# Optimization experiments

Measured on AMD Instinct MI355X. Metric: run time of the kernel, lower is better.

Reference implementation:

```python
import jax, jax.numpy as jnp
import numpy as np

BLOCK = 32          # per_1x32 microscaling block size along K
FP4_MAX = 6.0       # largest magnitude representable in e2m1
FP4_EMAX = 2.0      # exponent of largest fp4 binade (4..6)


def _quant_dequant_mxfp4(x):
    """Simulate MXFP4 (e2m1 elements, shared power-of-two E8M0 scale per 1x32
    block along the last dim): quantize then dequantize. x: [..., K], K % 32 == 0."""
    shape = x.shape
    xb = x.reshape(*shape[:-1], shape[-1] // BLOCK, BLOCK)
    amax = jnp.max(jnp.abs(xb), axis=-1, keepdims=True)
    # shared scale: 2^(floor(log2(amax)) - emax) so the block max lands in the top binade
    exp = jnp.floor(jnp.log2(jnp.maximum(amax, jnp.finfo(x.dtype).tiny))) - FP4_EMAX
    scale = jnp.where(amax > 0, jnp.exp2(exp), jnp.ones_like(amax))
    q = jnp.clip(xb / scale, -FP4_MAX, FP4_MAX)
    aq = jnp.abs(q)
    # e2m1 ulp: 0.5 on [0,2), 1 on [2,4), 2 on [4,6]
    lsb = jnp.where(aq < 2.0, 0.5, jnp.where(aq < 4.0, 1.0, 2.0))
    qr = jnp.round(q / lsb) * lsb  # round-to-nearest-even onto the fp4 grid
    return (qr * scale).reshape(shape)


def setup_inputs() -> dict:
    key = jax.random.key(0)
    k1, k2, k3 = jax.random.split(key, 3)
    B, S, K, N = 4, 2048, 2048, 2048
    inp = jax.random.normal(k1, (B, S, K), dtype=jnp.float32)
    weight = jax.random.normal(k2, (N, K), dtype=jnp.float32) * (1.0 / np.sqrt(K))
    bias = jax.random.normal(k3, (N,), dtype=jnp.float32) * 0.02
    return {"input": inp, "weight": weight, "bias": bias}


def reference(input, weight, bias):
    # both activation and weight are fake-quantized to MXFP4 per 1x32 blocks
    # along the contraction (in_features) dim, then a standard GEMM + bias.
    orig_shape = input.shape
    a = _quant_dequant_mxfp4(input.reshape(-1, orig_shape[-1]))  # [M, K]
    w = _quant_dequant_mxfp4(weight)                              # [N, K]
    out = jnp.einsum("mk,nk->mn", a, w) + bias
    return out.reshape(*orig_shape[:-1], weight.shape[0])
```

## Files before the change

### kernel.cpp

```cpp
#include <hip/hip_runtime.h>
#include <cstdint>


#define BM 128
#define BN 128
#define BK 256

typedef float floatx16 __attribute__((ext_vector_type(16)));
typedef int intx8 __attribute__((ext_vector_type(8)));

#define GLOBAL_AS __attribute__((address_space(1)))
#define LDS_AS __attribute__((address_space(3)))


__device__ __forceinline__ int enc1(float x, float inv) {
    float q = x * inv;
    q = fminf(fmaxf(q, -6.0f), 6.0f);
    int s = (int)(__float_as_uint(q) >> 31) << 3;
    float aq = fabsf(q);
    float ilsb = aq < 2.0f ? 2.0f : (aq < 4.0f ? 1.0f : 0.5f);
    float lsb  = aq < 2.0f ? 0.5f : (aq < 4.0f ? 1.0f : 2.0f);
    float ar = rintf(aq * ilsb) * lsb;
    int c;
    if (ar < 2.0f)      c = (int)(ar * 2.0f);
    else if (ar < 4.0f) c = 2 + (int)ar;
    else                c = 4 + (int)(ar * 0.5f);
    return c | s;
}

__global__ void quant_mxfp4_v4(const float* __restrict__ A, uint8_t* __restrict__ Aq,
                               uint8_t* __restrict__ AscT,
                               const float* __restrict__ W, uint8_t* __restrict__ Wq,
                               uint8_t* __restrict__ WscT,
                               long na4, long ntot4, int s4, long Mr, long Nr) {
    long t = (long)blockIdx.x * 256 + threadIdx.x;
    if (t >= ntot4) return;
    const float* src; uint8_t* dq; uint8_t* ds; long idx; long rows;
    if (t < na4) { src = A; dq = Aq; ds = AscT; idx = t; rows = Mr; }
    else         { src = W; dq = Wq; ds = WscT; idx = t - na4; rows = Nr; }

    float4 f = ((const float4*)src)[idx];
    float amax = fmaxf(fmaxf(fabsf(f.x), fabsf(f.y)),
                       fmaxf(fabsf(f.z), fabsf(f.w)));
    amax = fmaxf(amax, __shfl_xor(amax, 1));
    amax = fmaxf(amax, __shfl_xor(amax, 2));
    amax = fmaxf(amax, __shfl_xor(amax, 4));

    int ebits = (int)((__float_as_uint(amax) >> 23) & 0xff);
    int sb;
    float inv;
    if (amax > 0.0f) {
        sb = ebits - 2; if (sb < 0) sb = 0;
        inv = __uint_as_float((unsigned)((256 - ebits) & 255) << 23);
    } else {
        sb = 127;
        inv = 0.0f;
    }

    int c0 = enc1(f.x, inv), c1 = enc1(f.y, inv);
    int c2 = enc1(f.z, inv), c3 = enc1(f.w, inv);
    ((unsigned short*)dq)[idx] =
        (unsigned short)(c0 | (c1 << 4) | (c2 << 8) | (c3 << 12));
    if ((idx & 7) == 0) {
        long m  = idx >> s4;
        int  kb = (int)((idx & ((1L << s4) - 1)) >> 3);
        ds[(size_t)kb * rows + m] = (uint8_t)sb;
    }
}


__global__ __launch_bounds__(256, 2) void gemm_fp4_v8(
        const uint8_t* __restrict__ Aq, const uint8_t* __restrict__ AscT,
        const uint8_t* __restrict__ Wq, const uint8_t* __restrict__ WscT,
        const float* __restrict__ bias, float* __restrict__ C,
        int M, int N, int K) {
    __shared__ __align__(16) uint8_t sA[2][BM * 128];
    __shared__ __align__(16) uint8_t sB[2][BN * 128];

    const int tid = threadIdx.x;
    const int lane = tid & 63;
    const int w = tid >> 6;
    const int wr = w >> 1;
    const int wc = w & 1;
    const int row32 = lane & 31;
    const int q2 = lane >> 5;

    const int id = blockIdx.x;
    const int g = id & 7, h = id >> 3;
    const int by = g + 8 * (h & 7);
    const int bx = h >> 3;
    const int m0 = by * BM;
    const int n0 = bx * BN;
    const int KB2 = K >> 1;
    const int NT = K / BK;

    const int rA = wr * 64 + row32;
    const int rB = wc * 64 + row32;
    const int swz = row32 & 7;

    floatx16 acc[2][2];
#pragma unroll
    for (int i = 0; i < 2; i++)
#pragma unroll
        for (int j = 0; j < 2; j++)
#pragma unroll
            for (int r = 0; r < 16; r++) acc[i][j][r] = 0.f;

    auto stage = [&](int tt) {
        const int bb = tt & 1;
        const int kb = tt * 128;
#pragma unroll
        for (int it = 0; it < 4; ++it) {
            int idx = it * 256 + tid;
            int row = idx >> 3, c = idx & 7;
            int gc = c ^ (row & 7);
            const uint8_t* src = Aq + (size_t)(m0 + row) * KB2 + kb + gc * 16;
            __builtin_amdgcn_global_load_lds((GLOBAL_AS void*)src,
                (LDS_AS void*)(&sA[bb][idx * 16]), 16, 0, 0);
        }
#pragma unroll
        for (int it = 0; it < 4; ++it) {
            int idx = it * 256 + tid;
            int row = idx >> 3, c = idx & 7;
            int gc = c ^ (row & 7);
            const uint8_t* src = Wq + (size_t)(n0 + row) * KB2 + kb + gc * 16;
            __builtin_amdgcn_global_load_lds((GLOBAL_AS void*)src,
                (LDS_AS void*)(&sB[bb][idx * 16]), 16, 0, 0);
        }
    };

    stage(0);
    stage(1);
    asm volatile("s_waitcnt vmcnt(8)" ::: "memory");
    __builtin_amdgcn_sched_barrier(0);
    __builtin_amdgcn_s_barrier();

    for (int t = 0; t < NT; ++t) {
        const int p = t & 1;
        const uint8_t* pa = sA[p];
        const uint8_t* pb = sB[p];

        int sa[4][2], sb[4][2];
#pragma unroll
        for (int ks = 0; ks < 4; ++ks)
#pragma unroll
            for (int i = 0; i < 2; ++i) {
                sa[ks][i] = (int)AscT[(size_t)(8 * t + 2 * ks + q2) * M +
                                      m0 + wr * 64 + i * 32 + row32];
                sb[ks][i] = (int)WscT[(size_t)(8 * t + 2 * ks + q2) * N +
                                      n0 + wc * 64 + i * 32 + row32];
            }

        int4 fa[4][2], fb[4][2];
#pragma unroll
        for (int ks = 0; ks < 4; ++ks) {
            int off = ((ks * 2 + q2) ^ swz) * 16;
#pragma unroll
            for (int i = 0; i < 2; ++i) {
                fa[ks][i] = *(const int4*)(pa + (rA + i * 32) * 128 + off);
                fb[ks][i] = *(const int4*)(pb + (rB + i * 32) * 128 + off);
            }
        }

        asm volatile("s_waitcnt lgkmcnt(0)" ::: "memory");
        __builtin_amdgcn_sched_barrier(0);
        __builtin_amdgcn_s_barrier();

        if (t + 2 < NT) stage(t + 2);

        if (t + 2 < NT) asm volatile("s_waitcnt vmcnt(8)" ::: "memory");
        else            asm volatile("s_waitcnt vmcnt(0)" ::: "memory");
        __builtin_amdgcn_sched_barrier(0);

        __builtin_amdgcn_s_setprio(1);
#pragma unroll
        for (int ks = 0; ks < 4; ++ks) {
            intx8 a0, a1, b0, b1;
            a0[0] = fa[ks][0].x; a0[1] = fa[ks][0].y; a0[2] = fa[ks][0].z; a0[3] = fa[ks][0].w;
            a1[0] = fa[ks][1].x; a1[1] = fa[ks][1].y; a1[2] = fa[ks][1].z; a1[3] = fa[ks][1].w;
            b0[0] = fb[ks][0].x; b0[1] = fb[ks][0].y; b0[2] = fb[ks][0].z; b0[3] = fb[ks][0].w;
            b1[0] = fb[ks][1].x; b1[1] = fb[ks][1].y; b1[2] = fb[ks][1].z; b1[3] = fb[ks][1].w;
#pragma unroll
            for (int z = 4; z < 8; ++z) { a0[z] = 0; a1[z] = 0; b0[z] = 0; b1[z] = 0; }
            acc[0][0] = __builtin_amdgcn_mfma_scale_f32_32x32x64_f8f6f4(
                a0, b0, acc[0][0], 4, 4, 0, sa[ks][0], 0, sb[ks][0]);
            acc[0][1] = __builtin_amdgcn_mfma_scale_f32_32x32x64_f8f6f4(
                a0, b1, acc[0][1], 4, 4, 0, sa[ks][0], 0, sb[ks][1]);
            acc[1][0] = __builtin_amdgcn_mfma_scale_f32_32x32x64_f8f6f4(
                a1, b0, acc[1][0], 4, 4, 0, sa[ks][1], 0, sb[ks][0]);
            acc[1][1] = __builtin_amdgcn_mfma_scale_f32_32x32x64_f8f6f4(
                a1, b1, acc[1][1], 4, 4, 0, sa[ks][1], 0, sb[ks][1]);
        }
        __builtin_amdgcn_s_setprio(0);

        if (t < NT - 1) {
            if (t + 2 < NT) asm volatile("s_waitcnt vmcnt(8)" ::: "memory");
            else            asm volatile("s_waitcnt vmcnt(0)" ::: "memory");
            __builtin_amdgcn_sched_barrier(0);
            __builtin_amdgcn_s_barrier();
        }
    }

#pragma unroll
    for (int j = 0; j < 2; ++j) {
        int n = n0 + wc * 64 + j * 32 + row32;
        float bv = bias[n];
#pragma unroll
        for (int i = 0; i < 2; ++i) {
            int mb = m0 + wr * 64 + i * 32 + 4 * q2;
#pragma unroll
            for (int r = 0; r < 16; ++r) {
                int m = mb + (r & 3) + 8 * (r >> 2);
                C[(size_t)m * N + n] = acc[i][j][r] + bv;
            }
        }
    }
}


extern "C" void kernel_launch(void* const* d_in, const int* in_sizes, int n_in,
                              void* d_out, int out_size, void* d_ws, size_t ws_size,
                              hipStream_t stream) {
    const float* inp  = (const float*)d_in[0];
    const float* wgt  = (const float*)d_in[1];
    const float* bias = (const float*)d_in[2];
    float* out = (float*)d_out;

    const int N = in_sizes[2];
    const int K = in_sizes[1] / N;
    const long M = (long)in_sizes[0] / K;

    uint8_t* Aq4  = (uint8_t*)d_ws;
    uint8_t* Wq4  = Aq4 + (size_t)M * K / 2;
    uint8_t* AscT = Wq4 + (size_t)N * K / 2;
    uint8_t* WscT = AscT + (size_t)M * K / 32;

    int s4 = 0;
    while ((1 << s4) < (K >> 2)) ++s4;

    long na4   = (long)M * K / 4;
    long ntot4 = na4 + (long)N * K / 4;
    quant_mxfp4_v4<<<dim3((ntot4 + 255) / 256), dim3(256), 0, stream>>>(
        inp, Aq4, AscT, wgt, Wq4, WscT, na4, ntot4, s4, M, (long)N);

    dim3 grid((N / BN) * (int)(M / BM));
    gemm_fp4_v8<<<grid, dim3(256), 0, stream>>>(
        Aq4, AscT, Wq4, WscT, bias, out, (int)M, N, K);
}
```

Measured before the change: 152.6 us.

## Enlarge GEMM tile to 256x256 with 8 waves and packed scale layout

```diff
diff --git a/kernel.cpp b/kernel.cpp
--- a/kernel.cpp
+++ b/kernel.cpp
@@ -2,8 +2,8 @@
 #include <cstdint>
 
 
-#define BM 128
-#define BN 128
+#define BM 256
+#define BN 256
 #define BK 256
 
 typedef float floatx16 __attribute__((ext_vector_type(16)));
@@ -28,16 +28,16 @@
     return c | s;
 }
 
-__global__ void quant_mxfp4_v4(const float* __restrict__ A, uint8_t* __restrict__ Aq,
-                               uint8_t* __restrict__ AscT,
+__global__ void quant_mxfp4_v5(const float* __restrict__ A, uint8_t* __restrict__ Aq,
+                               uint8_t* __restrict__ Asc,
                                const float* __restrict__ W, uint8_t* __restrict__ Wq,
-                               uint8_t* __restrict__ WscT,
+                               uint8_t* __restrict__ Wsc,
                                long na4, long ntot4, int s4, long Mr, long Nr) {
     long t = (long)blockIdx.x * 256 + threadIdx.x;
     if (t >= ntot4) return;
     const float* src; uint8_t* dq; uint8_t* ds; long idx; long rows;
-    if (t < na4) { src = A; dq = Aq; ds = AscT; idx = t; rows = Mr; }
-    else         { src = W; dq = Wq; ds = WscT; idx = t - na4; rows = Nr; }
+    if (t < na4) { src = A; dq = Aq; ds = Asc; idx = t; rows = Mr; }
+    else         { src = W; dq = Wq; ds = Wsc; idx = t - na4; rows = Nr; }
 
     float4 f = ((const float4*)src)[idx];
     float amax = fmaxf(fmaxf(fabsf(f.x), fabsf(f.y)),
@@ -64,14 +64,83 @@
     if ((idx & 7) == 0) {
         long m  = idx >> s4;
         int  kb = (int)((idx & ((1L << s4) - 1)) >> 3);
-        ds[(size_t)kb * rows + m] = (uint8_t)sb;
-    }
-}
-
-
-__global__ __launch_bounds__(256, 2) void gemm_fp4_v8(
-        const uint8_t* __restrict__ Aq, const uint8_t* __restrict__ AscT,
-        const uint8_t* __restrict__ Wq, const uint8_t* __restrict__ WscT,
+        ds[((size_t)(kb >> 3) * rows + m) * 8 + (kb & 7)] = (uint8_t)sb;
+    }
+}
+
+
+#define GITER(T, CUR, NXT)                                                     \
+  {                                                                            \
+    const int p_ = (T) & 1;                                                    \
+    const uint8_t* pa_ = sA[p_];                                               \
+    const uint8_t* pb_ = sB[p_];                                               \
+    if ((T) + 1 < NT) {                                                        \
+      _Pragma("unroll") for (int mi = 0; mi < 4; ++mi)                         \
+        sgA[NXT][mi] = *(const uint2*)(Asc +                                   \
+            ((size_t)((T) + 1) * M + m0 + rA0 + mi * 32) * 8);                 \
+      _Pragma("unroll") for (int ni = 0; ni < 2; ++ni)                         \
+        sgB[NXT][ni] = *(const uint2*)(Wsc +                                   \
+            ((size_t)((T) + 1) * N + n0 + rB0 + ni * 32) * 8);                 \
+    }                                                                          \
+    __builtin_amdgcn_sched_barrier(0);                                         \
+    int4 fa_[4], fb_[2];                                                       \
+    _Pragma("unroll") for (int mi = 0; mi < 4; ++mi)                           \
+      fa_[mi] = *(const int4*)(pa_ + (rA0 + mi * 32) * 128 + (q2 ^ swz) * 16); \
+    _Pragma("unroll") for (int ni = 0; ni < 2; ++ni)                           \
+      fb_[ni] = *(const int4*)(pb_ + (rB0 + ni * 32) * 128 + (q2 ^ swz) * 16); \
+    __builtin_amdgcn_s_setprio(1);                                             \
+    _Pragma("unroll") for (int ks = 0; ks < 4; ++ks) {                         \
+      int4 na_[4], nb_[2];                                                     \
+      if (ks < 3) {                                                            \
+        const int off_ = (((ks + 1) * 2 + q2) ^ swz) * 16;                     \
+        _Pragma("unroll") for (int mi = 0; mi < 4; ++mi)                       \
+          na_[mi] = *(const int4*)(pa_ + (rA0 + mi * 32) * 128 + off_);        \
+        _Pragma("unroll") for (int ni = 0; ni < 2; ++ni)                       \
+          nb_[ni] = *(const int4*)(pb_ + (rB0 + ni * 32) * 128 + off_);        \
+      }                                                                        \
+      int sav_[4], sbv_[2];                                                    \
+      _Pragma("unroll") for (int mi = 0; mi < 4; ++mi)                         \
+        sav_[mi] = (int)(((ks < 2) ? (sgA[CUR][mi].x >> ((ks * 2 + q2) * 8))   \
+                   : (sgA[CUR][mi].y >> (((ks - 2) * 2 + q2) * 8))) & 0xffu);  \
+      _Pragma("unroll") for (int ni = 0; ni < 2; ++ni)                         \
+        sbv_[ni] = (int)(((ks < 2) ? (sgB[CUR][ni].x >> ((ks * 2 + q2) * 8))   \
+                   : (sgB[CUR][ni].y >> (((ks - 2) * 2 + q2) * 8))) & 0xffu);  \
+      intx8 b80_, b81_;                                                        \
+      b80_[0] = fb_[0].x; b80_[1] = fb_[0].y; b80_[2] = fb_[0].z;              \
+      b80_[3] = fb_[0].w; b80_[4] = 0; b80_[5] = 0; b80_[6] = 0; b80_[7] = 0;  \
+      b81_[0] = fb_[1].x; b81_[1] = fb_[1].y; b81_[2] = fb_[1].z;              \
+      b81_[3] = fb_[1].w; b81_[4] = 0; b81_[5] = 0; b81_[6] = 0; b81_[7] = 0;  \
+      _Pragma("unroll") for (int mi = 0; mi < 4; ++mi) {                       \
+        intx8 a8_;                                                             \
+        a8_[0] = fa_[mi].x; a8_[1] = fa_[mi].y; a8_[2] = fa_[mi].z;            \
+        a8_[3] = fa_[mi].w; a8_[4] = 0; a8_[5] = 0; a8_[6] = 0; a8_[7] = 0;    \
+        acc[mi][0] = __builtin_amdgcn_mfma_scale_f32_32x32x64_f8f6f4(          \
+            a8_, b80_, acc[mi][0], 4, 4, 0, sav_[mi], 0, sbv_[0]);             \
+        acc[mi][1] = __builtin_amdgcn_mfma_scale_f32_32x32x64_f8f6f4(          \
+            a8_, b81_, acc[mi][1], 4, 4, 0, sav_[mi], 0, sbv_[1]);             \
+      }                                                                        \
+      if (ks < 3) {                                                            \
+        _Pragma("unroll") for (int mi = 0; mi < 4; ++mi) fa_[mi] = na_[mi];    \
+        _Pragma("unroll") for (int ni = 0; ni < 2; ++ni) fb_[ni] = nb_[ni];    \
+      }                                                                        \
+    }                                                                          \
+    __builtin_amdgcn_s_setprio(0);                                             \
+    if ((T) + 1 < NT) {                                                        \
+      asm volatile("s_waitcnt lgkmcnt(0)" ::: "memory");                       \
+      __builtin_amdgcn_sched_barrier(0);                                       \
+      __builtin_amdgcn_s_barrier();                                            \
+      if ((T) + 2 < NT) stage((T) + 2);                                        \
+      __builtin_amdgcn_sched_barrier(0);                                       \
+      if ((T) + 2 < NT) asm volatile("s_waitcnt vmcnt(8)" ::: "memory");       \
+      else              asm volatile("s_waitcnt vmcnt(0)" ::: "memory");       \
+      __builtin_amdgcn_sched_barrier(0);                                       \
+      __builtin_amdgcn_s_barrier();                                            \
+    }                                                                          \
+  }
+
+__global__ __launch_bounds__(512, 2) void gemm_fp4_v9(
+        const uint8_t* __restrict__ Aq, const uint8_t* __restrict__ Asc,
+        const uint8_t* __restrict__ Wq, const uint8_t* __restrict__ Wsc,
         const float* __restrict__ bias, float* __restrict__ C,
         int M, int N, int K) {
     __shared__ __align__(16) uint8_t sA[2][BM * 128];
@@ -80,27 +149,27 @@
     const int tid = threadIdx.x;
     const int lane = tid & 63;
     const int w = tid >> 6;
-    const int wr = w >> 1;
-    const int wc = w & 1;
+    const int wr = w >> 2;
+    const int wc = w & 3;
     const int row32 = lane & 31;
     const int q2 = lane >> 5;
 
     const int id = blockIdx.x;
     const int g = id & 7, h = id >> 3;
-    const int by = g + 8 * (h & 7);
-    const int bx = h >> 3;
+    const int by = g * 4 + (h & 3);
+    const int bx = h >> 2;
     const int m0 = by * BM;
     const int n0 = bx * BN;
     const int KB2 = K >> 1;
     const int NT = K / BK;
 
-    const int rA = wr * 64 + row32;
-    const int rB = wc * 64 + row32;
+    const int rA0 = wr * 128 + row32;
+    const int rB0 = wc * 64 + row32;
     const int swz = row32 & 7;
 
-    floatx16 acc[2][2];
-#pragma unroll
-    for (int i = 0; i < 2; i++)
+    floatx16 acc[4][2];
+#pragma unroll
+    for (int i = 0; i < 4; i++)
 #pragma unroll
         for (int j = 0; j < 2; j++)
 #pragma unroll
@@ -111,7 +180,7 @@
         const int kb = tt * 128;
 #pragma unroll
         for (int it = 0; it < 4; ++it) {
-            int idx = it * 256 + tid;
+            int idx = it * 512 + tid;
             int row = idx >> 3, c = idx & 7;
             int gc = c ^ (row & 7);
             const uint8_t* src = Aq + (size_t)(m0 + row) * KB2 + kb + gc * 16;
@@ -120,7 +189,7 @@
         }
 #pragma unroll
         for (int it = 0; it < 4; ++it) {
-            int idx = it * 256 + tid;
+            int idx = it * 512 + tid;
             int row = idx >> 3, c = idx & 7;
             int gc = c ^ (row & 7);
             const uint8_t* src = Wq + (size_t)(n0 + row) * KB2 + kb + gc * 16;
@@ -129,89 +198,39 @@
         }
     };
 
+    uint2 sgA[2][4], sgB[2][2];
+
     stage(0);
+    __builtin_amdgcn_sched_barrier(0);
+#pragma unroll
+    for (int mi = 0; mi < 4; ++mi)
+        sgA[0][mi] = *(const uint2*)(Asc + ((size_t)0 * M + m0 + rA0 + mi * 32) * 8);
+#pragma unroll
+    for (int ni = 0; ni < 2; ++ni)
+        sgB[0][ni] = *(const uint2*)(Wsc + ((size_t)0 * N + n0 + rB0 + ni * 32) * 8);
+    __builtin_amdgcn_sched_barrier(0);
     stage(1);
+    __builtin_amdgcn_sched_barrier(0);
     asm volatile("s_waitcnt vmcnt(8)" ::: "memory");
     __builtin_amdgcn_sched_barrier(0);
     __builtin_amdgcn_s_barrier();
 
-    for (int t = 0; t < NT; ++t) {
-        const int p = t & 1;
-        const uint8_t* pa = sA[p];
-        const uint8_t* pb = sB[p];
-
-        int sa[4][2], sb[4][2];
-#pragma unroll
-        for (int ks = 0; ks < 4; ++ks)
-#pragma unroll
-            for (int i = 0; i < 2; ++i) {
-                sa[ks][i] = (int)AscT[(size_t)(8 * t + 2 * ks + q2) * M +
-                                      m0 + wr * 64 + i * 32 + row32];
-                sb[ks][i] = (int)WscT[(size_t)(8 * t + 2 * ks + q2) * N +
-                                      n0 + wc * 64 + i * 32 + row32];
-            }
-
-        int4 fa[4][2], fb[4][2];
-#pragma unroll
-        for (int ks = 0; ks < 4; ++ks) {
-            int off = ((ks * 2 + q2) ^ swz) * 16;
-#pragma unroll
-            for (int i = 0; i < 2; ++i) {
-                fa[ks][i] = *(const int4*)(pa + (rA + i * 32) * 128 + off);
-                fb[ks][i] = *(const int4*)(pb + (rB + i * 32) * 128 + off);
-            }
-        }
-
-        asm volatile("s_waitcnt lgkmcnt(0)" ::: "memory");
-        __builtin_amdgcn_sched_barrier(0);
-        __builtin_amdgcn_s_barrier();
-
-        if (t + 2 < NT) stage(t + 2);
-
-        if (t + 2 < NT) asm volatile("s_waitcnt vmcnt(8)" ::: "memory");
-        else            asm volatile("s_waitcnt vmcnt(0)" ::: "memory");
-        __builtin_amdgcn_sched_barrier(0);
-
-        __builtin_amdgcn_s_setprio(1);
-#pragma unroll
-        for (int ks = 0; ks < 4; ++ks) {
-            intx8 a0, a1, b0, b1;
-            a0[0] = fa[ks][0].x; a0[1] = fa[ks][0].y; a0[2] = fa[ks][0].z; a0[3] = fa[ks][0].w;
-            a1[0] = fa[ks][1].x; a1[1] = fa[ks][1].y; a1[2] = fa[ks][1].z; a1[3] = fa[ks][1].w;
-            b0[0] = fb[ks][0].x; b0[1] = fb[ks][0].y; b0[2] = fb[ks][0].z; b0[3] = fb[ks][0].w;
-            b1[0] = fb[ks][1].x; b1[1] = fb[ks][1].y; b1[2] = fb[ks][1].z; b1[3] = fb[ks][1].w;
-#pragma unroll
-            for (int z = 4; z < 8; ++z) { a0[z] = 0; a1[z] = 0; b0[z] = 0; b1[z] = 0; }
-            acc[0][0] = __builtin_amdgcn_mfma_scale_f32_32x32x64_f8f6f4(
-                a0, b0, acc[0][0], 4, 4, 0, sa[ks][0], 0, sb[ks][0]);
-            acc[0][1] = __builtin_amdgcn_mfma_scale_f32_32x32x64_f8f6f4(
-                a0, b1, acc[0][1], 4, 4, 0, sa[ks][0], 0, sb[ks][1]);
-            acc[1][0] = __builtin_amdgcn_mfma_scale_f32_32x32x64_f8f6f4(
-                a1, b0, acc[1][0], 4, 4, 0, sa[ks][1], 0, sb[ks][0]);
-            acc[1][1] = __builtin_amdgcn_mfma_scale_f32_32x32x64_f8f6f4(
-                a1, b1, acc[1][1], 4, 4, 0, sa[ks][1], 0, sb[ks][1]);
-        }
-        __builtin_amdgcn_s_setprio(0);
-
-        if (t < NT - 1) {
-            if (t + 2 < NT) asm volatile("s_waitcnt vmcnt(8)" ::: "memory");
-            else            asm volatile("s_waitcnt vmcnt(0)" ::: "memory");
-            __builtin_amdgcn_sched_barrier(0);
-            __builtin_amdgcn_s_barrier();
-        }
-    }
-
-#pragma unroll
-    for (int j = 0; j < 2; ++j) {
-        int n = n0 + wc * 64 + j * 32 + row32;
+    for (int t = 0; t < NT; t += 2) {
+        GITER(t, 0, 1);
+        GITER(t + 1, 1, 0);
+    }
+
+#pragma unroll
+    for (int ni = 0; ni < 2; ++ni) {
+        int n = n0 + wc * 64 + ni * 32 + row32;
         float bv = bias[n];
 #pragma unroll
-        for (int i = 0; i < 2; ++i) {
-            int mb = m0 + wr * 64 + i * 32 + 4 * q2;
+        for (int mi = 0; mi < 4; ++mi) {
+            int mb = m0 + wr * 128 + mi * 32 + 4 * q2;
 #pragma unroll
             for (int r = 0; r < 16; ++r) {
                 int m = mb + (r & 3) + 8 * (r >> 2);
-                C[(size_t)m * N + n] = acc[i][j][r] + bv;
+                C[(size_t)m * N + n] = acc[mi][ni][r] + bv;
             }
         }
     }
@@ -230,20 +249,20 @@
     const int K = in_sizes[1] / N;
     const long M = (long)in_sizes[0] / K;
 
-    uint8_t* Aq4  = (uint8_t*)d_ws;
-    uint8_t* Wq4  = Aq4 + (size_t)M * K / 2;
-    uint8_t* AscT = Wq4 + (size_t)N * K / 2;
-    uint8_t* WscT = AscT + (size_t)M * K / 32;
+    uint8_t* Aq4 = (uint8_t*)d_ws;
+    uint8_t* Wq4 = Aq4 + (size_t)M * K / 2;
+    uint8_t* Asc = Wq4 + (size_t)N * K / 2;
+    uint8_t* Wsc = Asc + (size_t)M * K / 32;
 
     int s4 = 0;
     while ((1 << s4) < (K >> 2)) ++s4;
 
     long na4   = (long)M * K / 4;
     long ntot4 = na4 + (long)N * K / 4;
-    quant_mxfp4_v4<<<dim3((ntot4 + 255) / 256), dim3(256), 0, stream>>>(
-        inp, Aq4, AscT, wgt, Wq4, WscT, na4, ntot4, s4, M, (long)N);
+    quant_mxfp4_v5<<<dim3((ntot4 + 255) / 256), dim3(256), 0, stream>>>(
+        inp, Aq4, Asc, wgt, Wq4, Wsc, na4, ntot4, s4, M, (long)N);
 
     dim3 grid((N / BN) * (int)(M / BM));
-    gemm_fp4_v8<<<grid, dim3(256), 0, stream>>>(
-        Aq4, AscT, Wq4, WscT, bias, out, (int)M, N, K);
-}
+    gemm_fp4_v9<<<grid, dim3(512), 0, stream>>>(
+        Aq4, Asc, Wq4, Wsc, bias, out, (int)M, N, K);
+}
```

Result: slower. 188.2 us (+23.3%).

## Pack per-tile scales into 8-byte groups and simplify GEMM pipeline

Applied to the files above, without the earlier changes.

```diff
diff --git a/kernel.cpp b/kernel.cpp
--- a/kernel.cpp
+++ b/kernel.cpp
@@ -28,16 +28,16 @@
     return c | s;
 }
 
-__global__ void quant_mxfp4_v4(const float* __restrict__ A, uint8_t* __restrict__ Aq,
-                               uint8_t* __restrict__ AscT,
+__global__ void quant_mxfp4_v5(const float* __restrict__ A, uint8_t* __restrict__ Aq,
+                               uint8_t* __restrict__ Asc,
                                const float* __restrict__ W, uint8_t* __restrict__ Wq,
-                               uint8_t* __restrict__ WscT,
+                               uint8_t* __restrict__ Wsc,
                                long na4, long ntot4, int s4, long Mr, long Nr) {
     long t = (long)blockIdx.x * 256 + threadIdx.x;
     if (t >= ntot4) return;
     const float* src; uint8_t* dq; uint8_t* ds; long idx; long rows;
-    if (t < na4) { src = A; dq = Aq; ds = AscT; idx = t; rows = Mr; }
-    else         { src = W; dq = Wq; ds = WscT; idx = t - na4; rows = Nr; }
+    if (t < na4) { src = A; dq = Aq; ds = Asc; idx = t; rows = Mr; }
+    else         { src = W; dq = Wq; ds = Wsc; idx = t - na4; rows = Nr; }
 
     float4 f = ((const float4*)src)[idx];
     float amax = fmaxf(fmaxf(fabsf(f.x), fabsf(f.y)),
@@ -64,14 +64,14 @@
     if ((idx & 7) == 0) {
         long m  = idx >> s4;
         int  kb = (int)((idx & ((1L << s4) - 1)) >> 3);
-        ds[(size_t)kb * rows + m] = (uint8_t)sb;
-    }
-}
-
-
-__global__ __launch_bounds__(256, 2) void gemm_fp4_v8(
-        const uint8_t* __restrict__ Aq, const uint8_t* __restrict__ AscT,
-        const uint8_t* __restrict__ Wq, const uint8_t* __restrict__ WscT,
+        ds[((size_t)(kb >> 3) * rows + m) * 8 + (kb & 7)] = (uint8_t)sb;
+    }
+}
+
+
+__global__ __launch_bounds__(256, 2) void gemm_fp4_v11(
+        const uint8_t* __restrict__ Aq, const uint8_t* __restrict__ Asc,
+        const uint8_t* __restrict__ Wq, const uint8_t* __restrict__ Wsc,
         const float* __restrict__ bias, float* __restrict__ C,
         int M, int N, int K) {
     __shared__ __align__(16) uint8_t sA[2][BM * 128];
@@ -130,75 +130,62 @@
     };
 
     stage(0);
-    stage(1);
-    asm volatile("s_waitcnt vmcnt(8)" ::: "memory");
-    __builtin_amdgcn_sched_barrier(0);
-    __builtin_amdgcn_s_barrier();
 
     for (int t = 0; t < NT; ++t) {
-        const int p = t & 1;
-        const uint8_t* pa = sA[p];
-        const uint8_t* pb = sB[p];
-
-        int sa[4][2], sb[4][2];
-#pragma unroll
-        for (int ks = 0; ks < 4; ++ks)
-#pragma unroll
-            for (int i = 0; i < 2; ++i) {
-                sa[ks][i] = (int)AscT[(size_t)(8 * t + 2 * ks + q2) * M +
-                                      m0 + wr * 64 + i * 32 + row32];
-                sb[ks][i] = (int)WscT[(size_t)(8 * t + 2 * ks + q2) * N +
-                                      n0 + wc * 64 + i * 32 + row32];
+        __syncthreads();
+        if (t + 1 < NT) stage(t + 1);
+
+        uint2 sga[2], sgb[2];
+#pragma unroll
+        for (int mi = 0; mi < 2; ++mi)
+            sga[mi] = *(const uint2*)(Asc + ((size_t)t * M + m0 + rA + mi * 32) * 8);
+#pragma unroll
+        for (int ni = 0; ni < 2; ++ni)
+            sgb[ni] = *(const uint2*)(Wsc + ((size_t)t * N + n0 + rB + ni * 32) * 8);
+
+        const uint8_t* pa = sA[t & 1];
+        const uint8_t* pb = sB[t & 1];
+
+#pragma unroll
+        for (int ks = 0; ks < 4; ++ks) {
+            const int off = ((ks * 2 + q2) ^ swz) * 16;
+            int4 fa0 = *(const int4*)(pa + (rA)      * 128 + off);
+            int4 fa1 = *(const int4*)(pa + (rA + 32) * 128 + off);
+            int4 fb0 = *(const int4*)(pb + (rB)      * 128 + off);
+            int4 fb1 = *(const int4*)(pb + (rB + 32) * 128 + off);
+
+            int sa0, sa1, sb0, sb1;
+            if (ks < 2) {
+                sa0 = (int)((sga[0].x >> ((ks * 2 + q2) * 8)) & 0xffu);
+                sa1 = (int)((sga[1].x >> ((ks * 2 + q2) * 8)) & 0xffu);
+                sb0 = (int)((sgb[0].x >> ((ks * 2 + q2) * 8)) & 0xffu);
+                sb1 = (int)((sgb[1].x >> ((ks * 2 + q2) * 8)) & 0xffu);
+            } else {
+                sa0 = (int)((sga[0].y >> (((ks - 2) * 2 + q2) * 8)) & 0xffu);
+                sa1 = (int)((sga[1].y >> (((ks - 2) * 2 + q2) * 8)) & 0xffu);
+                sb0 = (int)((sgb[0].y >> (((ks - 2) * 2 + q2) * 8)) & 0xffu);
+                sb1 = (int)((sgb[1].y >> (((ks - 2) * 2 + q2) * 8)) & 0xffu);
             }
 
-        int4 fa[4][2], fb[4][2];
-#pragma unroll
-        for (int ks = 0; ks < 4; ++ks) {
-            int off = ((ks * 2 + q2) ^ swz) * 16;
-#pragma unroll
-            for (int i = 0; i < 2; ++i) {
-                fa[ks][i] = *(const int4*)(pa + (rA + i * 32) * 128 + off);
-                fb[ks][i] = *(const int4*)(pb + (rB + i * 32) * 128 + off);
-            }
-        }
-
-        asm volatile("s_waitcnt lgkmcnt(0)" ::: "memory");
-        __builtin_amdgcn_sched_barrier(0);
-        __builtin_amdgcn_s_barrier();
-
-        if (t + 2 < NT) stage(t + 2);
-
-        if (t + 2 < NT) asm volatile("s_waitcnt vmcnt(8)" ::: "memory");
-        else            asm volatile("s_waitcnt vmcnt(0)" ::: "memory");
-        __builtin_amdgcn_sched_barrier(0);
-
-        __builtin_amdgcn_s_setprio(1);
-#pragma unroll
-        for (int ks = 0; ks < 4; ++ks) {
             intx8 a0, a1, b0, b1;
-            a0[0] = fa[ks][0].x; a0[1] = fa[ks][0].y; a0[2] = fa[ks][0].z; a0[3] = fa[ks][0].w;
-            a1[0] = fa[ks][1].x; a1[1] = fa[ks][1].y; a1[2] = fa[ks][1].z; a1[3] = fa[ks][1].w;
-            b0[0] = fb[ks][0].x; b0[1] = fb[ks][0].y; b0[2] = fb[ks][0].z; b0[3] = fb[ks][0].w;
-            b1[0] = fb[ks][1].x; b1[1] = fb[ks][1].y; b1[2] = fb[ks][1].z; b1[3] = fb[ks][1].w;
+            a0[0] = fa0.x; a0[1] = fa0.y; a0[2] = fa0.z; a0[3] = fa0.w;
+            a1[0] = fa1.x; a1[1] = fa1.y; a1[2] = fa1.z; a1[3] = fa1.w;
+            b0[0] = fb0.x; b0[1] = fb0.y; b0[2] = fb0.z; b0[3] = fb0.w;
+            b1[0] = fb1.x; b1[1] = fb1.y; b1[2] = fb1.z; b1[3] = fb1.w;
 #pragma unroll
             for (int z = 4; z < 8; ++z) { a0[z] = 0; a1[z] = 0; b0[z] = 0; b1[z] = 0; }
+
             acc[0][0] = __builtin_amdgcn_mfma_scale_f32_32x32x64_f8f6f4(
-                a0, b0, acc[0][0], 4, 4, 0, sa[ks][0], 0, sb[ks][0]);
+                a0, b0, acc[0][0], 4, 4, 0, sa0, 0, sb0);
             acc[0][1] = __builtin_amdgcn_mfma_scale_f32_32x32x64_f8f6f4(
-                a0, b1, acc[0][1], 4, 4, 0, sa[ks][0], 0, sb[ks][1]);
+                a0, b1, acc[0][1], 4, 4, 0, sa0, 0, sb1);
             acc[1][0] = __builtin_amdgcn_mfma_scale_f32_32x32x64_f8f6f4(
-                a1, b0, acc[1][0], 4, 4, 0, sa[ks][1], 0, sb[ks][0]);
+                a1, b0, acc[1][0], 4, 4, 0, sa1, 0, sb0);
             acc[1][1] = __builtin_amdgcn_mfma_scale_f32_32x32x64_f8f6f4(
-                a1, b1, acc[1][1], 4, 4, 0, sa[ks][1], 0, sb[ks][1]);
-        }
-        __builtin_amdgcn_s_setprio(0);
-
-        if (t < NT - 1) {
-            if (t + 2 < NT) asm volatile("s_waitcnt vmcnt(8)" ::: "memory");
-            else            asm volatile("s_waitcnt vmcnt(0)" ::: "memory");
-            __builtin_amdgcn_sched_barrier(0);
-            __builtin_amdgcn_s_barrier();
-        }
+                a1, b1, acc[1][1], 4, 4, 0, sa1, 0, sb1);
+        }
+
+        __syncthreads();
     }
 
 #pragma unroll
@@ -230,20 +217,20 @@
     const int K = in_sizes[1] / N;
     const long M = (long)in_sizes[0] / K;
 
-    uint8_t* Aq4  = (uint8_t*)d_ws;
-    uint8_t* Wq4  = Aq4 + (size_t)M * K / 2;
-    uint8_t* AscT = Wq4 + (size_t)N * K / 2;
-    uint8_t* WscT = AscT + (size_t)M * K / 32;
+    uint8_t* Aq4 = (uint8_t*)d_ws;
+    uint8_t* Wq4 = Aq4 + (size_t)M * K / 2;
+    uint8_t* Asc = Wq4 + (size_t)N * K / 2;
+    uint8_t* Wsc = Asc + (size_t)M * K / 32;
 
     int s4 = 0;
     while ((1 << s4) < (K >> 2)) ++s4;
 
     long na4   = (long)M * K / 4;
     long ntot4 = na4 + (long)N * K / 4;
-    quant_mxfp4_v4<<<dim3((ntot4 + 255) / 256), dim3(256), 0, stream>>>(
-        inp, Aq4, AscT, wgt, Wq4, WscT, na4, ntot4, s4, M, (long)N);
+    quant_mxfp4_v5<<<dim3((ntot4 + 255) / 256), dim3(256), 0, stream>>>(
+        inp, Aq4, Asc, wgt, Wq4, Wsc, na4, ntot4, s4, M, (long)N);
 
     dim3 grid((N / BN) * (int)(M / BM));
-    gemm_fp4_v8<<<grid, dim3(256), 0, stream>>>(
-        Aq4, AscT, Wq4, WscT, bias, out, (int)M, N, K);
-}
+    gemm_fp4_v11<<<grid, dim3(256), 0, stream>>>(
+        Aq4, Asc, Wq4, Wsc, bias, out, (int)M, N, K);
+}
```

Result: no change. 152.7 us (+0.0%).
